# Kernel optimization log

Measured on AMD Instinct MI355X. Metric: run time of the kernel, lower is better.

The kernel has to match this reference:

```python
import jax, jax.numpy as jnp
import numpy as np

B, T, D, H = 2, 2048, 1024, 4
DK, DV = 1024, 2048          # key_dim = d_model*expand_k, value_dim = d_model*expand_v
HK, HV = DK // H, DV // H    # 256, 512 per-head dims
LR = 16                      # gate_low_rank_dim
EPS = 1e-5
GATE_NORM = 16.0             # gate_logit_normalizer


def _xavier(k, shape, gain):
    fan_in, fan_out = shape
    lim = gain * np.sqrt(6.0 / (fan_in + fan_out))
    return jax.random.uniform(k, shape, jnp.float32, -lim, lim)


def setup_inputs() -> dict:
    key = jax.random.key(0)
    ks = jax.random.split(key, 10)
    g_qkv = 2 ** (-2.5)
    return {
        "x": jax.random.normal(ks[0], (B, T, D), jnp.float32),
        "Wq": _xavier(ks[1], (D, DK), g_qkv),
        "Wk": _xavier(ks[2], (D, DK), g_qkv),
        "Wv": _xavier(ks[3], (D, DV), g_qkv),
        "Wg": _xavier(ks[4], (D, DV), g_qkv),
        "gk_w1": _xavier(ks[5], (D, LR), g_qkv),
        "gk_w2": _xavier(ks[6], (LR, DK), g_qkv),
        "gk_b": jnp.zeros((DK,), jnp.float32),
        "Wo": _xavier(ks[7], (DV, D), 2 ** (-1)),
        "rms_w": jnp.ones((HV,), jnp.float32),
    }


def _gla_scan(q, k, v, g):
    # q,k,g: [T, hk]; v: [T, hv]. Recurrence S_t = diag(exp(g_t)) S_{t-1} + k_t v_t^T; o_t = q_t @ S_t
    S0 = jnp.zeros((q.shape[-1], v.shape[-1]), q.dtype)

    def step(S, inp):
        qt, kt, vt, gt = inp
        S = jnp.exp(gt)[:, None] * S + kt[:, None] * vt[None, :]
        return S, qt @ S

    return jax.lax.scan(step, S0, (q, k, v, g))[1]  # [T, hv]


def _forward(x, Wq, Wk, Wv, Wg, gk_w1, gk_w2, gk_b, Wo, rms_w):
    b, t = x.shape[0], x.shape[1]
    scale = HK ** -0.5
    # projections -> [b, h, t, d_head]
    q = (x @ Wq).reshape(b, t, H, HK).transpose(0, 2, 1, 3) * scale
    k = (x @ Wk).reshape(b, t, H, HK).transpose(0, 2, 1, 3)
    v = (x @ Wv).reshape(b, t, H, HV).transpose(0, 2, 1, 3)
    # low-rank forget gate, log-space, fp32
    gl = (x @ gk_w1) @ gk_w2 + gk_b
    g = (jax.nn.log_sigmoid(gl.astype(jnp.float32)) / GATE_NORM)
    g = g.reshape(b, t, H, HK).transpose(0, 2, 1, 3)
    # per-(batch, head) linear-attention recurrence
    o = jax.vmap(jax.vmap(_gla_scan))(q, k, v, g)  # [b, h, t, hv]
    # group RMSNorm over head_v_dim
    o = o.transpose(0, 2, 1, 3)  # [b, t, h, hv]
    o = o * jax.lax.rsqrt(jnp.mean(o * o, axis=-1, keepdims=True) + EPS) * rms_w
    # output gate (swish) + out projection
    o = o.reshape(b, t, DV) * jax.nn.silu(x @ Wg)
    return o @ Wo  # [b, t, d_model]


def reference(x, Wq, Wk, Wv, Wg, gk_w1, gk_w2, gk_b, Wo, rms_w):
    return _forward(x, Wq, Wk, Wv, Wg, gk_w1, gk_w2, gk_b, Wo, rms_w)
```

## Files before the change

### kernel.cpp

```cpp
#include <hip/hip_runtime.h>
#include <cstdint>
#include <cstddef>


typedef unsigned short u16;
typedef __attribute__((ext_vector_type(8))) short s8v;
typedef __attribute__((ext_vector_type(4))) short s4v;
typedef __attribute__((ext_vector_type(4))) float f4v;

__device__ __forceinline__ u16 f2b(float f) {
  unsigned u = __builtin_bit_cast(unsigned, f);
  unsigned r = u + 0x7FFFu + ((u >> 16) & 1u);
  return (u16)(r >> 16);
}
__device__ __forceinline__ float b2f(u16 h) {
  unsigned u = ((unsigned)h) << 16;
  return __builtin_bit_cast(float, u);
}

__device__ __forceinline__ void cp16(const void* g, void* l) {
  __builtin_amdgcn_global_load_lds(
      (const __attribute__((address_space(1))) unsigned int*)g,
      (__attribute__((address_space(3))) unsigned int*)l, 16, 0, 0);
}

__device__ __forceinline__ void stage_tile(const u16* g, int ld, u16* lds,
                                           int wv, int ln) {
  const int q = (ln & 3) ^ ((ln >> 3) & 3);
#pragma unroll
  for (int i = 0; i < 2; ++i) {
    const int c = wv * 2 + i;
    const u16* src = g + (size_t)(c * 16 + (ln >> 2)) * ld + q * 8;
    cp16(src, lds + c * 512);
  }
}

__device__ __forceinline__ void gemm_core(
    const u16* __restrict__ A, int lda, const u16* __restrict__ BT, int ldb,
    int K, u16* As, u16* Bs, f4v acc[4][4])
{
  const int tid = threadIdx.x;
  const int ln = tid & 63, wv = tid >> 6;
  const int arow = (wv >> 1) * 64 + (ln & 15);
  const int brow = (wv & 1) * 64 + (ln & 15);
  const int koff = (((ln >> 4) ^ ((ln >> 1) & 3)) * 8);
  const int nt = K >> 5;
  stage_tile(A, lda, As, wv, ln);
  stage_tile(BT, ldb, Bs, wv, ln);
  stage_tile(A + 32, lda, As + 4096, wv, ln);
  stage_tile(BT + 32, ldb, Bs + 4096, wv, ln);
  int slot = 0;
  for (int t = 0; t < nt; ++t) {
    if (t + 1 < nt) asm volatile("s_waitcnt vmcnt(4)" ::: "memory");
    else            asm volatile("s_waitcnt vmcnt(0)" ::: "memory");
    __builtin_amdgcn_s_barrier();
    __builtin_amdgcn_sched_barrier(0);
    const u16* Ab = As + slot * 4096;
    const u16* Bb = Bs + slot * 4096;
    s8v af[4], bf[4];
#pragma unroll
    for (int f = 0; f < 4; ++f)
      af[f] = *(const s8v*)(Ab + (arow + f * 16) * 32 + koff);
#pragma unroll
    for (int f = 0; f < 4; ++f)
      bf[f] = *(const s8v*)(Bb + (brow + f * 16) * 32 + koff);
#pragma unroll
    for (int mf = 0; mf < 4; ++mf)
#pragma unroll
      for (int nf = 0; nf < 4; ++nf)
        acc[mf][nf] = __builtin_amdgcn_mfma_f32_16x16x32_bf16(
            af[mf], bf[nf], acc[mf][nf], 0, 0, 0);
    __builtin_amdgcn_sched_barrier(0);
    __builtin_amdgcn_s_barrier();
    if (t + 2 < nt) {
      stage_tile(A + (t + 2) * 32, lda, As + slot * 4096, wv, ln);
      stage_tile(BT + (t + 2) * 32, ldb, Bs + slot * 4096, wv, ln);
    }
    slot ^= 1;
  }
}

__device__ __forceinline__ void frag_to_lds(u16* S, const f4v acc[4][4],
                                            int ln, int wv) {
  u16* q = S + wv * 4608;
#pragma unroll
  for (int mf = 0; mf < 4; ++mf)
#pragma unroll
    for (int nf = 0; nf < 4; ++nf)
#pragma unroll
      for (int r = 0; r < 4; ++r)
        q[(mf * 16 + ((ln >> 4) << 2) + r) * 72 + nf * 16 + (ln & 15)] =
            f2b(acc[mf][nf][r]);
}

__device__ __forceinline__ void frag_to_lds_T(u16* S, const f4v acc[4][4],
                                              int ln, int wv) {
  const int wr = wv >> 1, wc = wv & 1;
  u16* q = S + ((wc << 1) + wr) * 4608;
#pragma unroll
  for (int mf = 0; mf < 4; ++mf)
#pragma unroll
    for (int nf = 0; nf < 4; ++nf) {
      const int cl = nf * 16 + (ln & 15);
      const int rl = mf * 16 + ((ln >> 4) << 2);
      s4v o4;
#pragma unroll
      for (int r = 0; r < 4; ++r) o4[r] = (short)f2b(acc[mf][nf][r]);
      *(s4v*)(q + cl * 72 + rl) = o4;
    }
}

template <typename F>
__device__ __forceinline__ void epi_loop(u16* S, const f4v acc[4][4], F f) {
  const int tid = threadIdx.x;
  frag_to_lds(S, acc, tid & 63, tid >> 6);
  __syncthreads();
#pragma unroll
  for (int p = 0; p < 8; ++p) {
    const int r = p * 16 + (tid >> 4);
    const int c0 = (tid & 15) * 8;
    const int quad = ((r >> 6) << 1) + (c0 >> 6);
    s8v vv = *(const s8v*)(S + quad * 4608 + (r & 63) * 72 + (c0 & 63));
    f(r, c0, vv);
  }
}

template <typename F>
__device__ __forceinline__ void epi_loop_T(u16* S, const f4v acc[4][4], F f) {
  const int tid = threadIdx.x;
  frag_to_lds_T(S, acc, tid & 63, tid >> 6);
  __syncthreads();
#pragma unroll
  for (int p = 0; p < 8; ++p) {
    const int r = p * 16 + (tid >> 4);
    const int c0 = (tid & 15) * 8;
    const int quad = ((r >> 6) << 1) + (c0 >> 6);
    s8v vv = *(const s8v*)(S + quad * 4608 + (r & 63) * 72 + (c0 & 63));
    f(r, c0, vv);
  }
}

__global__ __launch_bounds__(256) void castw_all(
    const float* __restrict__ x, const float* __restrict__ Wq,
    const float* __restrict__ Wk, const float* __restrict__ Wv,
    const float* __restrict__ Wg, const float* __restrict__ Wo,
    u16* __restrict__ xb, u16* __restrict__ WTa, u16* __restrict__ WoT)
{
  __shared__ float t[32][33];
  const int id = blockIdx.x;
  if (id < 4096) {
    const int i = id * 256 + threadIdx.x;
    const float4 v = ((const float4*)x)[i];
    u16* p = xb + i * 4;
    p[0] = f2b(v.x); p[1] = f2b(v.y); p[2] = f2b(v.z); p[3] = f2b(v.w);
    return;
  }
  const int wid = id - 4096;
  const float* src; u16* dst; int R, C, local;
  if (wid < 1024)      { src = Wq; dst = WTa;           R = 1024; C = 1024; local = wid; }
  else if (wid < 2048) { src = Wk; dst = WTa + 1048576; R = 1024; C = 1024; local = wid - 1024; }
  else if (wid < 4096) { src = Wv; dst = WTa + 2097152; R = 1024; C = 2048; local = wid - 2048; }
  else if (wid < 6144) { src = Wg; dst = WTa + 4194304; R = 1024; C = 2048; local = wid - 4096; }
  else                 { src = Wo; dst = WoT;           R = 2048; C = 1024; local = wid - 6144; }
  const int nx = C >> 5;
  const int c0 = (local % nx) * 32, r0 = (local / nx) * 32;
  const int lx = threadIdx.x & 31, ly = threadIdx.x >> 5;
#pragma unroll
  for (int i = 0; i < 32; i += 8)
    t[ly + i][lx] = src[(size_t)(r0 + ly + i) * C + c0 + lx];
  __syncthreads();
#pragma unroll
  for (int i = 0; i < 32; i += 8)
    dst[(size_t)(c0 + ly + i) * R + r0 + lx] = f2b(t[lx][ly + i]);
}

__global__ __launch_bounds__(256) void trans_kt(
    const u16* __restrict__ kt, u16* __restrict__ ktT)
{
  __shared__ u16 t[32][33];
  const int id = blockIdx.x;
  const int z = id >> 9, local = id & 511;
  const int c0 = (local & 7) * 32, r0 = (local >> 3) * 32;
  const size_t boff = (size_t)z * 2048 * 256;
  const int lx = threadIdx.x & 31, ly = threadIdx.x >> 5;
#pragma unroll
  for (int i = 0; i < 32; i += 8)
    t[ly + i][lx] = kt[boff + (size_t)(r0 + ly + i) * 256 + c0 + lx];
  __syncthreads();
#pragma unroll
  for (int i = 0; i < 32; i += 8)
    ktT[boff + (size_t)(c0 + ly + i) * 2048 + r0 + lx] = t[lx][ly + i];
}

__global__ __launch_bounds__(256) void lowrank1(
    const float* __restrict__ x, const float* __restrict__ w1,
    float* __restrict__ tmp)
{
  const int idx = blockIdx.x * 256 + threadIdx.x;
  const int m = idx >> 4, i = idx & 15;
  const float* xr = x + (size_t)m * 1024;
  float acc = 0.f;
#pragma unroll 4
  for (int kk = 0; kk < 1024; kk += 4) {
    const float4 xv = *(const float4*)(xr + kk);
    acc = fmaf(xv.x, w1[(kk + 0) * 16 + i], acc);
    acc = fmaf(xv.y, w1[(kk + 1) * 16 + i], acc);
    acc = fmaf(xv.z, w1[(kk + 2) * 16 + i], acc);
    acc = fmaf(xv.w, w1[(kk + 3) * 16 + i], acc);
  }
  tmp[idx] = acc;
}

__global__ __launch_bounds__(256) void gate_cum(
    const float* __restrict__ tmp, const float* __restrict__ w2,
    const float* __restrict__ bias, u16* __restrict__ dq, u16* __restrict__ dk,
    float* __restrict__ Dc)
{
  __shared__ float ls_t[2048];
  const int b = blockIdx.y >> 4, c = blockIdx.y & 15;
  const int h = blockIdx.x;
  const int i = threadIdx.x;
  const int n = h * 256 + i;
  const int bh = b * 4 + h;
  const float* tp = tmp + ((size_t)(b * 2048 + c * 128)) * 16;
#pragma unroll
  for (int r = 0; r < 8; ++r) ls_t[r * 256 + threadIdx.x] = tp[r * 256 + threadIdx.x];
  __syncthreads();
  float w2c[16];
#pragma unroll
  for (int r = 0; r < 16; ++r) w2c[r] = w2[r * 1024 + n];
  const float bn = bias[n];
  const size_t base = ((size_t)bh * 2048 + c * 128) * 256 + i;
  float B = 0.f;
  for (int t = 0; t < 128; ++t) {
    float gl = bn;
    const float* tr = ls_t + t * 16;
#pragma unroll
    for (int r = 0; r < 16; ++r) gl = fmaf(tr[r], w2c[r], gl);
    const float ls = fminf(gl, 0.f) - log1pf(expf(-fabsf(gl)));
    B += ls * 0.0625f;
    const float eB = expf(B);
    dq[base + (size_t)t * 256] = f2b(eB);
    dk[base + (size_t)t * 256] = f2b(1.f / eB);
  }
  Dc[(bh * 16 + c) * 256 + i] = expf(B);
}

__global__ __launch_bounds__(256) void proj_all(
    const u16* __restrict__ xb, const u16* __restrict__ WT,
    const u16* __restrict__ dq, const u16* __restrict__ dk,
    u16* __restrict__ qt, u16* __restrict__ kt,
    u16* __restrict__ vT, u16* __restrict__ gpre)
{
  __shared__ __align__(16) u16 S[18432];
  u16* As = S; u16* Bs = S + 8192;
  const int id = blockIdx.x;
  const int xcd = id & 7, jb = id >> 3;
  const int m0 = (jb / 6) * 128;
  const int n0 = (xcd * 6 + (jb % 6)) * 128;
  f4v acc[4][4];
#pragma unroll
  for (int zi = 0; zi < 4; ++zi)
#pragma unroll
    for (int zj = 0; zj < 4; ++zj) acc[zi][zj] = (f4v){0.f, 0.f, 0.f, 0.f};
  gemm_core(xb + (size_t)m0 * 1024, 1024, WT + (size_t)n0 * 1024, 1024, 1024,
            As, Bs, acc);
  const int bb = m0 >> 11;
  const int t0 = m0 & 2047;
  if (n0 < 1024) {
    epi_loop(S, acc, [&](int r, int c0, s8v vv) {
      const int t = t0 + r;
      const int n = n0 + c0;
      const int bh = bb * 4 + (n >> 8);
      const size_t off = ((size_t)bh * 2048 + t) * 256 + (n & 255);
      const s8v dv = *(const s8v*)(dq + off);
      s8v o8;
#pragma unroll
      for (int e = 0; e < 8; ++e)
        o8[e] = (short)f2b(b2f((u16)vv[e]) * 0.0625f * b2f((u16)dv[e]));
      *(s8v*)(qt + off) = o8;
    });
  } else if (n0 < 2048) {
    epi_loop(S, acc, [&](int r, int c0, s8v vv) {
      const int t = t0 + r;
      const int nn = n0 + c0 - 1024;
      const int bh = bb * 4 + (nn >> 8);
      const size_t off = ((size_t)bh * 2048 + t) * 256 + (nn & 255);
      const s8v dv = *(const s8v*)(dk + off);
      s8v o8;
#pragma unroll
      for (int e = 0; e < 8; ++e)
        o8[e] = (short)f2b(b2f((u16)vv[e]) * b2f((u16)dv[e]));
      *(s8v*)(kt + off) = o8;
    });
  } else if (n0 < 4096) {
    const int nn0 = n0 - 2048;
    const int bh = bb * 4 + (nn0 >> 9);
    const int jj0 = nn0 & 511;
    epi_loop_T(S, acc, [&](int r, int c0, s8v vv) {
      *(s8v*)(vT + ((size_t)(bh * 512 + jj0 + r)) * 2048 + t0 + c0) = vv;
    });
  } else {
    epi_loop(S, acc, [&](int r, int c0, s8v vv) {
      *(s8v*)(gpre + (size_t)(m0 + r) * 2048 + (n0 + c0 - 4096)) = vv;
    });
  }
}

__global__ __launch_bounds__(256) void scan_gemms(
    const u16* __restrict__ vT, const u16* __restrict__ ktT,
    const u16* __restrict__ qt, const u16* __restrict__ kt,
    u16* __restrict__ UT, u16* __restrict__ Aw)
{
  __shared__ __align__(16) u16 S[18432];
  u16* As = S; u16* Bs = S + 8192;
  const int bhc = blockIdx.y, bh = bhc >> 4, c = bhc & 15;
  f4v acc[4][4];
#pragma unroll
  for (int zi = 0; zi < 4; ++zi)
#pragma unroll
    for (int zj = 0; zj < 4; ++zj) acc[zi][zj] = (f4v){0.f, 0.f, 0.f, 0.f};
  if (blockIdx.x < 8) {
    const int mt = blockIdx.x >> 1, nt = blockIdx.x & 1;
    gemm_core(vT + ((size_t)bh * 512 + mt * 128) * 2048 + c * 128, 2048,
              ktT + ((size_t)bh * 256 + nt * 128) * 2048 + c * 128, 2048, 128,
              As, Bs, acc);
    epi_loop(S, acc, [&](int r, int c0, s8v vv) {
      const int j = mt * 128 + r;
      const int i = nt * 128 + c0;
      *(s8v*)(UT + (((size_t)(bh * 512 + j)) * 16 + c) * 256 + i) = vv;
    });
  } else {
    const size_t base = ((size_t)bh * 2048 + c * 128) * 256;
    gemm_core(qt + base, 256, kt + base, 256, 256, As, Bs, acc);
    u16* Ap = Aw + (size_t)bhc * 16384;
    epi_loop(S, acc, [&](int r, int c0, s8v vv) {
      s8v o8;
#pragma unroll
      for (int e = 0; e < 8; ++e)
        o8[e] = (c0 + e <= r) ? vv[e] : (short)0;
      *(s8v*)(Ap + r * 128 + c0) = o8;
    });
  }
}

__global__ __launch_bounds__(256) void state_scan(
    u16* __restrict__ UT, const float* __restrict__ Dc)
{
  const int blk = blockIdx.x;
  const int bh = blk >> 9, j = blk & 511;
  const int i = threadIdx.x;
  u16* Up = UT + ((size_t)(bh * 512 + j)) * 16 * 256 + i;
  const float* Dp = Dc + bh * 16 * 256 + i;
  float Sa = 0.f;
#pragma unroll
  for (int c = 0; c < 16; ++c) {
    const float u = b2f(Up[c * 256]);
    const float d = Dp[c * 256];
    Up[c * 256] = f2b(Sa);
    Sa = d * (Sa + u);
  }
}

__global__ __launch_bounds__(256) void intra_k(
    const u16* __restrict__ Aw, const u16* __restrict__ qt,
    const u16* __restrict__ vT, const u16* __restrict__ UT, u16* __restrict__ ob)
{
  __shared__ __align__(16) u16 S[18432];
  u16* As = S; u16* Bs = S + 8192;
  const int jt = blockIdx.x;
  const int bhc = blockIdx.y, bh = bhc >> 4, c = bhc & 15;
  f4v acc[4][4];
#pragma unroll
  for (int zi = 0; zi < 4; ++zi)
#pragma unroll
    for (int zj = 0; zj < 4; ++zj) acc[zi][zj] = (f4v){0.f, 0.f, 0.f, 0.f};
  gemm_core(Aw + (size_t)bhc * 16384, 128,
            vT + ((size_t)bh * 512 + jt * 128) * 2048 + c * 128, 2048, 128,
            As, Bs, acc);
  gemm_core(qt + ((size_t)bh * 2048 + c * 128) * 256, 256,
            UT + ((size_t)(bh * 512 + jt * 128)) * 4096 + (size_t)c * 256, 4096, 256,
            As, Bs, acc);
  const int b = bh >> 2, h = bh & 3;
  epi_loop(S, acc, [&](int r, int c0, s8v vv) {
    const int t = c * 128 + r;
    const int j = jt * 128 + c0;
    *(s8v*)(ob + ((size_t)(b * 2048 + t)) * 2048 + h * 512 + j) = vv;
  });
}

__global__ __launch_bounds__(256) void rms_silu(
    u16* __restrict__ o, const u16* __restrict__ gpre, const float* __restrict__ w)
{
  const int grp = blockIdx.x * 4 + (threadIdx.x >> 6);
  const int lane = threadIdx.x & 63;
  const size_t base = (size_t)(grp >> 2) * 2048 + (grp & 3) * 512 + lane * 8;
  const s8v xv = *(const s8v*)(o + base);
  float xf[8];
  float ss = 0.f;
#pragma unroll
  for (int i = 0; i < 8; ++i) {
    xf[i] = b2f((u16)xv[i]);
    ss = fmaf(xf[i], xf[i], ss);
  }
#pragma unroll
  for (int off = 1; off < 64; off <<= 1) ss += __shfl_xor(ss, off, 64);
  const float r = rsqrtf(ss * (1.f / 512.f) + 1e-5f);
  const s8v gv = *(const s8v*)(gpre + base);
  const float4 w0 = *(const float4*)(w + lane * 8);
  const float4 w1 = *(const float4*)(w + lane * 8 + 4);
  const float wf[8] = {w0.x, w0.y, w0.z, w0.w, w1.x, w1.y, w1.z, w1.w};
  s8v o8;
#pragma unroll
  for (int i = 0; i < 8; ++i) {
    const float gp = b2f((u16)gv[i]);
    const float sig = 1.f / (1.f + expf(-gp));
    o8[i] = (short)f2b(xf[i] * r * wf[i] * gp * sig);
  }
  *(s8v*)(o + base) = o8;
}

__global__ __launch_bounds__(256) void gemm_out(
    const u16* __restrict__ ob, const u16* __restrict__ WoT,
    float* __restrict__ pout)
{
  __shared__ __align__(16) u16 S[18432];
  u16* As = S; u16* Bs = S + 8192;
  const int id = blockIdx.x;
  const int wg = (id & 7) * 64 + (id >> 3);
  const int ks = wg >> 8;
  const int tt = wg & 255;
  const int m0 = (tt & 31) * 128, n0 = (tt >> 5) * 128;
  f4v acc[4][4];
#pragma unroll
  for (int zi = 0; zi < 4; ++zi)
#pragma unroll
    for (int zj = 0; zj < 4; ++zj) acc[zi][zj] = (f4v){0.f, 0.f, 0.f, 0.f};
  gemm_core(ob + (size_t)m0 * 2048 + ks * 1024, 2048,
            WoT + (size_t)n0 * 2048 + ks * 1024, 2048, 1024, As, Bs, acc);
  const int tid = threadIdx.x;
  const int ln = tid & 63, wv = tid >> 6;
  const int wr = wv >> 1, wc = wv & 1;
  float* po = pout + (size_t)ks * 4194304;
#pragma unroll
  for (int mf = 0; mf < 4; ++mf)
#pragma unroll
    for (int nf = 0; nf < 4; ++nf)
#pragma unroll
      for (int r = 0; r < 4; ++r) {
        const int m = m0 + wr * 64 + mf * 16 + ((ln >> 4) << 2) + r;
        const int n = n0 + wc * 64 + nf * 16 + (ln & 15);
        po[(size_t)m * 1024 + n] = acc[mf][nf][r];
      }
}

__global__ __launch_bounds__(256) void reduce_out(
    const float* __restrict__ p, float* __restrict__ out)
{
  const int i = blockIdx.x * 256 + threadIdx.x;
  const float4 a = ((const float4*)p)[i];
  const float4 b = ((const float4*)(p + 4194304))[i];
  ((float4*)out)[i] = make_float4(a.x + b.x, a.y + b.y, a.z + b.z, a.w + b.w);
}

extern "C" void kernel_launch(void* const* d_in, const int* in_sizes, int n_in,
                              void* d_out, int out_size, void* d_ws, size_t ws_size,
                              hipStream_t stream) {
  const float* x    = (const float*)d_in[0];
  const float* Wq   = (const float*)d_in[1];
  const float* Wk   = (const float*)d_in[2];
  const float* Wv   = (const float*)d_in[3];
  const float* Wg   = (const float*)d_in[4];
  const float* w1   = (const float*)d_in[5];
  const float* w2   = (const float*)d_in[6];
  const float* gb   = (const float*)d_in[7];
  const float* Wo   = (const float*)d_in[8];
  const float* rmsw = (const float*)d_in[9];
  float* out = (float*)d_out;

  char* W = (char*)d_ws;
  u16*   xb   = (u16*)W;   W += (size_t)8  << 20;
  u16*   WTa  = (u16*)W;   W += (size_t)12 << 20;
  u16*   WoT  = (u16*)W;   W += (size_t)4  << 20;
  u16*   qt   = (u16*)W;   W += (size_t)8  << 20;
  u16*   kt   = (u16*)W;   W += (size_t)8  << 20;
  u16*   vT   = (u16*)W;   W += (size_t)16 << 20;
  u16*   ktT  = (u16*)W;   W += (size_t)8  << 20;
  u16*   gpre = (u16*)W;   W += (size_t)16 << 20;
  float* tmp  = (float*)W; W += (size_t)256 << 10;
  float* Dc   = (float*)W; W += (size_t)128 << 10;
  u16*   dq   = (u16*)W;   W += (size_t)8  << 20;
  u16*   dk   = (u16*)W;   W += (size_t)8  << 20;
  u16*   UT   = (u16*)W;   W += (size_t)32 << 20;
  u16*   Aw   = (u16*)W;   W += (size_t)4  << 20;
  u16*   ob   = (u16*)W;   W += (size_t)16 << 20;
  float* pout = (float*)W; W += (size_t)32 << 20;

  hipLaunchKernelGGL(lowrank1, dim3(256), dim3(256), 0, stream, x, w1, tmp);
  hipLaunchKernelGGL(gate_cum, dim3(4, 32), dim3(256), 0, stream,
                     tmp, w2, gb, dq, dk, Dc);

  hipLaunchKernelGGL(castw_all, dim3(12288), dim3(256), 0, stream,
                     x, Wq, Wk, Wv, Wg, Wo, xb, WTa, WoT);

  hipLaunchKernelGGL(proj_all, dim3(1536), dim3(256), 0, stream,
                     xb, WTa, dq, dk, qt, kt, vT, gpre);

  hipLaunchKernelGGL(trans_kt, dim3(4096), dim3(256), 0, stream, kt, ktT);

  hipLaunchKernelGGL(scan_gemms, dim3(9, 128), dim3(256), 0, stream,
                     vT, ktT, qt, kt, UT, Aw);
  hipLaunchKernelGGL(state_scan, dim3(4096), dim3(256), 0, stream, UT, Dc);
  hipLaunchKernelGGL(intra_k, dim3(4, 128), dim3(256), 0, stream, Aw, qt, vT, UT, ob);

  hipLaunchKernelGGL(rms_silu, dim3(4096), dim3(256), 0, stream, ob, gpre, rmsw);
  hipLaunchKernelGGL(gemm_out, dim3(512), dim3(256), 0, stream, ob, WoT, pout);
  hipLaunchKernelGGL(reduce_out, dim3(4096), dim3(256), 0, stream, pout, out);
}
```

Measured before the change: 261.3 us.

## Fuse x bf16 cast into lowrank1, split gate_cum blocks, merge intra GEMM pipelines

```diff
diff --git a/kernel.cpp b/kernel.cpp
--- a/kernel.cpp
+++ b/kernel.cpp
@@ -80,6 +80,58 @@
   }
 }
 
+__device__ __forceinline__ void gemm_core2(
+    const u16* __restrict__ A1, int lda1, const u16* __restrict__ B1, int ldb1,
+    int K1,
+    const u16* __restrict__ A2, int lda2, const u16* __restrict__ B2, int ldb2,
+    int K2, u16* As, u16* Bs, f4v acc[4][4])
+{
+  const int tid = threadIdx.x;
+  const int ln = tid & 63, wv = tid >> 6;
+  const int arow = (wv >> 1) * 64 + (ln & 15);
+  const int brow = (wv & 1) * 64 + (ln & 15);
+  const int koff = (((ln >> 4) ^ ((ln >> 1) & 3)) * 8);
+  const int nt1 = K1 >> 5;
+  const int nt = nt1 + (K2 >> 5);
+  auto stage_step = [&](int t, int slot) {
+    if (t < nt1) {
+      stage_tile(A1 + t * 32, lda1, As + slot * 4096, wv, ln);
+      stage_tile(B1 + t * 32, ldb1, Bs + slot * 4096, wv, ln);
+    } else {
+      stage_tile(A2 + (t - nt1) * 32, lda2, As + slot * 4096, wv, ln);
+      stage_tile(B2 + (t - nt1) * 32, ldb2, Bs + slot * 4096, wv, ln);
+    }
+  };
+  stage_step(0, 0);
+  stage_step(1, 1);
+  int slot = 0;
+  for (int t = 0; t < nt; ++t) {
+    if (t + 1 < nt) asm volatile("s_waitcnt vmcnt(4)" ::: "memory");
+    else            asm volatile("s_waitcnt vmcnt(0)" ::: "memory");
+    __builtin_amdgcn_s_barrier();
+    __builtin_amdgcn_sched_barrier(0);
+    const u16* Ab = As + slot * 4096;
+    const u16* Bb = Bs + slot * 4096;
+    s8v af[4], bf[4];
+#pragma unroll
+    for (int f = 0; f < 4; ++f)
+      af[f] = *(const s8v*)(Ab + (arow + f * 16) * 32 + koff);
+#pragma unroll
+    for (int f = 0; f < 4; ++f)
+      bf[f] = *(const s8v*)(Bb + (brow + f * 16) * 32 + koff);
+#pragma unroll
+    for (int mf = 0; mf < 4; ++mf)
+#pragma unroll
+      for (int nf = 0; nf < 4; ++nf)
+        acc[mf][nf] = __builtin_amdgcn_mfma_f32_16x16x32_bf16(
+            af[mf], bf[nf], acc[mf][nf], 0, 0, 0);
+    __builtin_amdgcn_sched_barrier(0);
+    __builtin_amdgcn_s_barrier();
+    if (t + 2 < nt) stage_step(t + 2, slot);
+    slot ^= 1;
+  }
+}
+
 __device__ __forceinline__ void frag_to_lds(u16* S, const f4v acc[4][4],
                                             int ln, int wv) {
   u16* q = S + wv * 4608;
@@ -141,21 +193,13 @@
 }
 
 __global__ __launch_bounds__(256) void castw_all(
-    const float* __restrict__ x, const float* __restrict__ Wq,
-    const float* __restrict__ Wk, const float* __restrict__ Wv,
-    const float* __restrict__ Wg, const float* __restrict__ Wo,
-    u16* __restrict__ xb, u16* __restrict__ WTa, u16* __restrict__ WoT)
+    const float* __restrict__ Wq, const float* __restrict__ Wk,
+    const float* __restrict__ Wv, const float* __restrict__ Wg,
+    const float* __restrict__ Wo,
+    u16* __restrict__ WTa, u16* __restrict__ WoT)
 {
   __shared__ float t[32][33];
-  const int id = blockIdx.x;
-  if (id < 4096) {
-    const int i = id * 256 + threadIdx.x;
-    const float4 v = ((const float4*)x)[i];
-    u16* p = xb + i * 4;
-    p[0] = f2b(v.x); p[1] = f2b(v.y); p[2] = f2b(v.z); p[3] = f2b(v.w);
-    return;
-  }
-  const int wid = id - 4096;
+  const int wid = blockIdx.x;
   const float* src; u16* dst; int R, C, local;
   if (wid < 1024)      { src = Wq; dst = WTa;           R = 1024; C = 1024; local = wid; }
   else if (wid < 2048) { src = Wk; dst = WTa + 1048576; R = 1024; C = 1024; local = wid - 1024; }
@@ -194,7 +238,7 @@
 
 __global__ __launch_bounds__(256) void lowrank1(
     const float* __restrict__ x, const float* __restrict__ w1,
-    float* __restrict__ tmp)
+    float* __restrict__ tmp, u16* __restrict__ xb)
 {
   const int idx = blockIdx.x * 256 + threadIdx.x;
   const int m = idx >> 4, i = idx & 15;
@@ -209,22 +253,37 @@
     acc = fmaf(xv.w, w1[(kk + 3) * 16 + i], acc);
   }
   tmp[idx] = acc;
-}
-
-__global__ __launch_bounds__(256) void gate_cum(
+  const float* xs = xr + i * 64;
+  u16* xo = xb + (size_t)m * 1024 + i * 64;
+#pragma unroll
+  for (int p = 0; p < 8; ++p) {
+    const float4 a = *(const float4*)(xs + p * 8);
+    const float4 b = *(const float4*)(xs + p * 8 + 4);
+    s8v o8;
+    o8[0] = (short)f2b(a.x); o8[1] = (short)f2b(a.y);
+    o8[2] = (short)f2b(a.z); o8[3] = (short)f2b(a.w);
+    o8[4] = (short)f2b(b.x); o8[5] = (short)f2b(b.y);
+    o8[6] = (short)f2b(b.z); o8[7] = (short)f2b(b.w);
+    *(s8v*)(xo + p * 8) = o8;
+  }
+}
+
+__global__ __launch_bounds__(64) void gate_cum(
     const float* __restrict__ tmp, const float* __restrict__ w2,
     const float* __restrict__ bias, u16* __restrict__ dq, u16* __restrict__ dk,
     float* __restrict__ Dc)
 {
   __shared__ float ls_t[2048];
   const int b = blockIdx.y >> 4, c = blockIdx.y & 15;
-  const int h = blockIdx.x;
-  const int i = threadIdx.x;
+  const int h = blockIdx.x >> 2;
+  const int iq = blockIdx.x & 3;
+  const int lane = threadIdx.x;
+  const int i = iq * 64 + lane;
   const int n = h * 256 + i;
   const int bh = b * 4 + h;
   const float* tp = tmp + ((size_t)(b * 2048 + c * 128)) * 16;
 #pragma unroll
-  for (int r = 0; r < 8; ++r) ls_t[r * 256 + threadIdx.x] = tp[r * 256 + threadIdx.x];
+  for (int r = 0; r < 32; ++r) ls_t[r * 64 + lane] = tp[r * 64 + lane];
   __syncthreads();
   float w2c[16];
 #pragma unroll
@@ -375,12 +434,11 @@
   for (int zi = 0; zi < 4; ++zi)
 #pragma unroll
     for (int zj = 0; zj < 4; ++zj) acc[zi][zj] = (f4v){0.f, 0.f, 0.f, 0.f};
-  gemm_core(Aw + (size_t)bhc * 16384, 128,
-            vT + ((size_t)bh * 512 + jt * 128) * 2048 + c * 128, 2048, 128,
-            As, Bs, acc);
-  gemm_core(qt + ((size_t)bh * 2048 + c * 128) * 256, 256,
-            UT + ((size_t)(bh * 512 + jt * 128)) * 4096 + (size_t)c * 256, 4096, 256,
-            As, Bs, acc);
+  gemm_core2(Aw + (size_t)bhc * 16384, 128,
+             vT + ((size_t)bh * 512 + jt * 128) * 2048 + c * 128, 2048, 128,
+             qt + ((size_t)bh * 2048 + c * 128) * 256, 256,
+             UT + ((size_t)(bh * 512 + jt * 128)) * 4096 + (size_t)c * 256,
+             4096, 256, As, Bs, acc);
   const int b = bh >> 2, h = bh & 3;
   epi_loop(S, acc, [&](int r, int c0, s8v vv) {
     const int t = c * 128 + r;
@@ -496,12 +554,12 @@
   u16*   ob   = (u16*)W;   W += (size_t)16 << 20;
   float* pout = (float*)W; W += (size_t)32 << 20;
 
-  hipLaunchKernelGGL(lowrank1, dim3(256), dim3(256), 0, stream, x, w1, tmp);
-  hipLaunchKernelGGL(gate_cum, dim3(4, 32), dim3(256), 0, stream,
+  hipLaunchKernelGGL(lowrank1, dim3(256), dim3(256), 0, stream, x, w1, tmp, xb);
+  hipLaunchKernelGGL(gate_cum, dim3(16, 32), dim3(64), 0, stream,
                      tmp, w2, gb, dq, dk, Dc);
 
-  hipLaunchKernelGGL(castw_all, dim3(12288), dim3(256), 0, stream,
-                     x, Wq, Wk, Wv, Wg, Wo, xb, WTa, WoT);
+  hipLaunchKernelGGL(castw_all, dim3(8192), dim3(256), 0, stream,
+                     Wq, Wk, Wv, Wg, Wo, WTa, WoT);
 
   hipLaunchKernelGGL(proj_all, dim3(1536), dim3(256), 0, stream,
                      xb, WTa, dq, dk, qt, kt, vT, gpre);
```

Result: slower. 268.5 us (+2.8%).
